# Kernel tuning notes

Measured on AMD Instinct MI355X. Metric: run time of the kernel, lower is better.

## Reference

```python
import jax, jax.numpy as jnp
import numpy as np
import math

B, C, H, W = 16, 256, 128, 128
N = 4096
D = 256  # out_channels
IMG = 512


def _bilinear_sample(features, grid):
    """features (B,C,H,W), grid (B,N,2) in [-1,1] (x,y). align_corners=True, border padding."""
    Bq, Cq, Hq, Wq = features.shape
    ix = (grid[..., 0] + 1.0) * 0.5 * (Wq - 1)  # (B,N)
    iy = (grid[..., 1] + 1.0) * 0.5 * (Hq - 1)
    # border padding: clamp continuous coords into valid range
    ix = jnp.clip(ix, 0.0, Wq - 1)
    iy = jnp.clip(iy, 0.0, Hq - 1)
    x0 = jnp.floor(ix)
    y0 = jnp.floor(iy)
    wx = ix - x0
    wy = iy - y0
    x0i = jnp.clip(x0.astype(jnp.int32), 0, Wq - 1)
    y0i = jnp.clip(y0.astype(jnp.int32), 0, Hq - 1)
    x1i = jnp.clip(x0i + 1, 0, Wq - 1)
    y1i = jnp.clip(y0i + 1, 0, Hq - 1)
    f = features.reshape(Bq, Cq, Hq * Wq)

    def gather(yi, xi):
        idx = (yi * Wq + xi)[:, None, :]  # (B,1,N)
        return jnp.take_along_axis(f, idx, axis=2)  # (B,C,N)

    v00 = gather(y0i, x0i)
    v01 = gather(y0i, x1i)
    v10 = gather(y1i, x0i)
    v11 = gather(y1i, x1i)
    wx = wx[:, None, :]
    wy = wy[:, None, :]
    top = v00 * (1 - wx) + v01 * wx
    bot = v10 * (1 - wx) + v11 * wx
    return top * (1 - wy) + bot * wy  # (B,C,N)


def _pos_encoding(positions, d_model):
    """positions (B,N,2) in [0,1] -> (B,N,2*d_model) sinusoidal."""
    div_term = jnp.exp(jnp.arange(0, d_model, 2, dtype=jnp.float32)
                       * (-math.log(10000.0) / d_model))  # (d_model//2,)
    x = positions[..., 0:1] * 1000.0  # (B,N,1)
    y = positions[..., 1:2] * 1000.0

    def interleave(v):
        a = v * div_term  # (B,N,d_model//2)
        sc = jnp.stack([jnp.sin(a), jnp.cos(a)], axis=-1)  # (B,N,d//2,2)
        return sc.reshape(*v.shape[:-1], d_model)

    return jnp.concatenate([interleave(x), interleave(y)], axis=-1)


def setup_inputs() -> dict:
    key = jax.random.key(0)
    ks = jax.random.split(key, 8)
    features = jax.random.normal(ks[0], (B, C, H, W), dtype=jnp.float32)
    vertices = jax.random.uniform(ks[1], (B, N, 2), dtype=jnp.float32) * IMG
    s1 = 1.0 / math.sqrt(C)
    s2 = 1.0 / math.sqrt(D)
    W1 = jax.random.uniform(ks[2], (C, D), jnp.float32, -s1, s1)
    b1 = jnp.zeros((D,), jnp.float32)
    W2 = jax.random.uniform(ks[3], (D, D), jnp.float32, -s2, s2)
    b2 = jnp.zeros((D,), jnp.float32)
    Wp = jax.random.uniform(ks[4], (D, D), jnp.float32, -s2, s2)
    bp = jnp.zeros((D,), jnp.float32)
    return {"features": features, "vertices": vertices, "image_size": IMG,
            "W1": W1, "b1": b1, "W2": W2, "b2": b2, "Wp": Wp, "bp": bp}


def reference(features, vertices, image_size, W1, b1, W2, b2, Wp, bp):
    # normalize pixel coords to [-1,1] (align_corners=True convention)
    denom = jnp.float32(image_size - 1)
    grid = 2.0 * vertices / denom - 1.0  # (B,N,2)
    sampled = _bilinear_sample(features, grid)  # (B,C,N)
    sampled = jnp.transpose(sampled, (0, 2, 1))  # (B,N,C)
    h = jax.nn.relu(jnp.einsum('bnc,cd->bnd', sampled, W1) + b1)
    vfeat = jnp.einsum('bnd,de->bne', h, W2) + b2  # (B,N,D)
    pos_enc = _pos_encoding(vertices / jnp.float32(image_size), D // 2)  # (B,N,D)
    out = jnp.einsum('bnd,de->bne', vfeat + pos_enc, Wp) + bp
    return out
```

## Files before the change

### kernel.cpp

```cpp
#include <hip/hip_runtime.h>

#define HW 16384
#define Nn 4096

typedef __bf16 bf16x8 __attribute__((ext_vector_type(8)));
typedef unsigned short us8t __attribute__((ext_vector_type(8)));
typedef float f32x4 __attribute__((ext_vector_type(4)));

__device__ __forceinline__ unsigned short f2bf(float f) {
    unsigned int u = __float_as_uint(f);
    u = (u + 0x7fffu + ((u >> 16) & 1u)) >> 16;
    return (unsigned short)u;
}
__device__ __forceinline__ float bf2f(unsigned int h) {
    return __uint_as_float(h << 16);
}
__device__ __forceinline__ f32x4 mfma16(us8t a, us8t b, f32x4 c) {
    return __builtin_amdgcn_mfma_f32_16x16x32_bf16(
        __builtin_bit_cast(bf16x8, a), __builtin_bit_cast(bf16x8, b), c, 0, 0, 0);
}

__global__ __launch_bounds__(256) void k_wt(const float* __restrict__ W1,
                                            const float* __restrict__ W2,
                                            const float* __restrict__ Wp,
                                            unsigned short* __restrict__ WT) {
    const int m = blockIdx.x >> 8;
    const int d = blockIdx.x & 255;
    const int c = threadIdx.x;
    const float* W = (m == 0) ? W1 : (m == 1) ? W2 : Wp;
    WT[m * 65536 + d * 256 + c] = f2bf(W[c * 256 + d]);
}

__global__ __launch_bounds__(256) void k_gemm1(const float* __restrict__ f,
                                               const unsigned short* __restrict__ W1T,
                                               unsigned short* __restrict__ S, int b0) {
    __shared__ __align__(16) unsigned short Asb[64][40];

    const int blk = blockIdx.x;
    const int bl = blk >> 8;
    const int b = b0 + bl;
    const int p0 = (blk & 255) << 6;
    const int t = threadIdx.x;
    const int lane = t & 63;
    const int w = t >> 6;
    const int sc = t >> 4;
    const int sp = (t & 15) << 2;
    const int mrow = lane & 15;
    const int kg = (lane >> 4) << 3;
    const int n0w = w << 6;

    const float* fb = f + ((size_t)b << 22);

    f32x4 acc[4][4];
#pragma unroll
    for (int i = 0; i < 4; ++i)
#pragma unroll
        for (int j = 0; j < 4; ++j) acc[i][j] = (f32x4){0.f, 0.f, 0.f, 0.f};

    us8t bnx[4];
#pragma unroll
    for (int nt = 0; nt < 4; ++nt)
        bnx[nt] = *(const us8t*)(W1T + ((n0w + (nt << 4) + mrow) << 8) + kg);

    for (int k0 = 0; k0 < 256; k0 += 32) {
        __syncthreads();
#pragma unroll
        for (int it = 0; it < 2; ++it) {
            const int c = sc + (it << 4);
            const float4 v = *(const float4*)(fb + ((size_t)(k0 + c) << 14) + p0 + sp);
            Asb[sp + 0][c] = f2bf(v.x);
            Asb[sp + 1][c] = f2bf(v.y);
            Asb[sp + 2][c] = f2bf(v.z);
            Asb[sp + 3][c] = f2bf(v.w);
        }
        us8t bcur[4];
#pragma unroll
        for (int nt = 0; nt < 4; ++nt) bcur[nt] = bnx[nt];
        if (k0 < 224) {
#pragma unroll
            for (int nt = 0; nt < 4; ++nt)
                bnx[nt] = *(const us8t*)(W1T + ((n0w + (nt << 4) + mrow) << 8) + k0 + 32 + kg);
        }
        __syncthreads();
        us8t af[4];
#pragma unroll
        for (int mt = 0; mt < 4; ++mt)
            af[mt] = *(const us8t*)&Asb[(mt << 4) + mrow][kg];
#pragma unroll
        for (int mt = 0; mt < 4; ++mt)
#pragma unroll
            for (int nt = 0; nt < 4; ++nt)
                acc[mt][nt] = mfma16(af[mt], bcur[nt], acc[mt][nt]);
    }

    unsigned short* Sp = S + ((((size_t)bl << 14) + p0) << 8);
    const int r0 = (lane >> 4) << 2;
#pragma unroll
    for (int mt = 0; mt < 4; ++mt)
#pragma unroll
        for (int nt = 0; nt < 4; ++nt) {
            const int col = n0w + (nt << 4) + mrow;
#pragma unroll
            for (int j = 0; j < 4; ++j) {
                const int row = (mt << 4) + r0 + j;
                Sp[((size_t)row << 8) + col] = f2bf(acc[mt][nt][j]);
            }
        }
}

__global__ __launch_bounds__(256) void k_fused(const unsigned short* __restrict__ S,
                                               const float* __restrict__ verts,
                                               const int* __restrict__ iszp,
                                               const unsigned short* __restrict__ W2T,
                                               const unsigned short* __restrict__ WpT,
                                               const float* __restrict__ b1,
                                               const float* __restrict__ b2,
                                               const float* __restrict__ bpv,
                                               float* __restrict__ out, int b0) {
    __shared__ __align__(16) unsigned short hT[64][264];
    __shared__ __align__(16) int pIdx[64][4];
    __shared__ __align__(16) float wBl[64][4];
    __shared__ float vps[64][2];
    __shared__ __align__(16) float b1s[256];
    __shared__ float b2s[256], bps[256];

    const int blk = blockIdx.x;
    const int bl = blk >> 6;
    const int b = b0 + bl;
    const int n0 = (blk & 63) << 6;
    const int t = threadIdx.x;
    const int lane = t & 63;
    const int w = t >> 6;

    b1s[t] = b1[t];
    b2s[t] = b2[t];
    bps[t] = bpv[t];

    if (t < 64) {
        const float isz = (float)iszp[0];
        const size_t vo = ((size_t)b * Nn + n0 + t) << 1;
        const float vx = verts[vo + 0];
        const float vy = verts[vo + 1];
        const float gs = 127.0f / (isz - 1.0f);
        const float ix = fminf(fmaxf(vx * gs, 0.0f), 127.0f);
        const float iy = fminf(fmaxf(vy * gs, 0.0f), 127.0f);
        const float x0 = floorf(ix), y0 = floorf(iy);
        const float wx = ix - x0, wy = iy - y0;
        const int x0i = (int)x0, y0i = (int)y0;
        const int x1i = min(x0i + 1, 127), y1i = min(y0i + 1, 127);
        pIdx[t][0] = (y0i << 7) + x0i;
        pIdx[t][1] = (y0i << 7) + x1i;
        pIdx[t][2] = (y1i << 7) + x0i;
        pIdx[t][3] = (y1i << 7) + x1i;
        wBl[t][0] = (1.0f - wx) * (1.0f - wy);
        wBl[t][1] = wx * (1.0f - wy);
        wBl[t][2] = (1.0f - wx) * wy;
        wBl[t][3] = wx * wy;
        vps[t][0] = vx / isz;
        vps[t][1] = vy / isz;
    }
    __syncthreads();

    {
        const unsigned short* Sb = S + ((size_t)bl << 22);
        const float4 bl1 = *(const float4*)&b1s[lane << 2];
        for (int i = 0; i < 16; ++i) {
            const int r = (w << 4) + i;
            const int4 pp = *(const int4*)pIdx[r];
            const float4 wt = *(const float4*)wBl[r];
            const uint2 a0 = *(const uint2*)(Sb + ((size_t)pp.x << 8) + (lane << 2));
            const uint2 a1 = *(const uint2*)(Sb + ((size_t)pp.y << 8) + (lane << 2));
            const uint2 a2 = *(const uint2*)(Sb + ((size_t)pp.z << 8) + (lane << 2));
            const uint2 a3 = *(const uint2*)(Sb + ((size_t)pp.w << 8) + (lane << 2));
            float d0 = wt.x * bf2f(a0.x & 0xffffu) + wt.y * bf2f(a1.x & 0xffffu) +
                       wt.z * bf2f(a2.x & 0xffffu) + wt.w * bf2f(a3.x & 0xffffu) + bl1.x;
            float d1 = wt.x * bf2f(a0.x >> 16) + wt.y * bf2f(a1.x >> 16) +
                       wt.z * bf2f(a2.x >> 16) + wt.w * bf2f(a3.x >> 16) + bl1.y;
            float d2 = wt.x * bf2f(a0.y & 0xffffu) + wt.y * bf2f(a1.y & 0xffffu) +
                       wt.z * bf2f(a2.y & 0xffffu) + wt.w * bf2f(a3.y & 0xffffu) + bl1.z;
            float d3 = wt.x * bf2f(a0.y >> 16) + wt.y * bf2f(a1.y >> 16) +
                       wt.z * bf2f(a2.y >> 16) + wt.w * bf2f(a3.y >> 16) + bl1.w;
            d0 = fmaxf(d0, 0.0f);
            d1 = fmaxf(d1, 0.0f);
            d2 = fmaxf(d2, 0.0f);
            d3 = fmaxf(d3, 0.0f);
            uint2 pk;
            pk.x = (unsigned)f2bf(d0) | ((unsigned)f2bf(d1) << 16);
            pk.y = (unsigned)f2bf(d2) | ((unsigned)f2bf(d3) << 16);
            *(uint2*)&hT[r][lane << 2] = pk;
        }
    }
    __syncthreads();

    const int mrow = lane & 15;
    const int kg = (lane >> 4) << 3;
    const int r0 = (lane >> 4) << 2;
    const int n0w = w << 6;

    f32x4 acc[4][4];
#pragma unroll
    for (int i = 0; i < 4; ++i)
#pragma unroll
        for (int j = 0; j < 4; ++j) acc[i][j] = (f32x4){0.f, 0.f, 0.f, 0.f};

    us8t bnx[4];
#pragma unroll
    for (int nt = 0; nt < 4; ++nt)
        bnx[nt] = *(const us8t*)(W2T + ((n0w + (nt << 4) + mrow) << 8) + kg);
    for (int k0 = 0; k0 < 256; k0 += 32) {
        us8t bcur[4];
#pragma unroll
        for (int nt = 0; nt < 4; ++nt) bcur[nt] = bnx[nt];
        if (k0 < 224) {
#pragma unroll
            for (int nt = 0; nt < 4; ++nt)
                bnx[nt] = *(const us8t*)(W2T + ((n0w + (nt << 4) + mrow) << 8) + k0 + 32 + kg);
        }
        us8t af[4];
#pragma unroll
        for (int mt = 0; mt < 4; ++mt)
            af[mt] = *(const us8t*)&hT[(mt << 4) + mrow][k0 + kg];
#pragma unroll
        for (int mt = 0; mt < 4; ++mt)
#pragma unroll
            for (int nt = 0; nt < 4; ++nt)
                acc[mt][nt] = mfma16(af[mt], bcur[nt], acc[mt][nt]);
    }
    __syncthreads();

    const float C2 = -0.20762050593046f;
#pragma unroll
    for (int nt = 0; nt < 4; ++nt) {
        const int col = n0w + (nt << 4) + mrow;
        const float bias2 = b2s[col];
        const int ci = col & 127;
        const float dv = exp2f((float)(ci >> 1) * C2) * 1000.0f;
        const int sel = col >> 7;
#pragma unroll
        for (int mt = 0; mt < 4; ++mt)
#pragma unroll
            for (int j = 0; j < 4; ++j) {
                const int row = (mt << 4) + r0 + j;
                const float ang = vps[row][sel] * dv;
                const float pe = (col & 1) ? __cosf(ang) : __sinf(ang);
                hT[row][col] = f2bf(acc[mt][nt][j] + bias2 + pe);
            }
    }
    __syncthreads();

#pragma unroll
    for (int i = 0; i < 4; ++i)
#pragma unroll
        for (int j = 0; j < 4; ++j) acc[i][j] = (f32x4){0.f, 0.f, 0.f, 0.f};
#pragma unroll
    for (int nt = 0; nt < 4; ++nt)
        bnx[nt] = *(const us8t*)(WpT + ((n0w + (nt << 4) + mrow) << 8) + kg);
    for (int k0 = 0; k0 < 256; k0 += 32) {
        us8t bcur[4];
#pragma unroll
        for (int nt = 0; nt < 4; ++nt) bcur[nt] = bnx[nt];
        if (k0 < 224) {
#pragma unroll
            for (int nt = 0; nt < 4; ++nt)
                bnx[nt] = *(const us8t*)(WpT + ((n0w + (nt << 4) + mrow) << 8) + k0 + 32 + kg);
        }
        us8t af[4];
#pragma unroll
        for (int mt = 0; mt < 4; ++mt)
            af[mt] = *(const us8t*)&hT[(mt << 4) + mrow][k0 + kg];
#pragma unroll
        for (int mt = 0; mt < 4; ++mt)
#pragma unroll
            for (int nt = 0; nt < 4; ++nt)
                acc[mt][nt] = mfma16(af[mt], bcur[nt], acc[mt][nt]);
    }

    float* ob = out + (((size_t)b * Nn + n0) << 8);
#pragma unroll
    for (int nt = 0; nt < 4; ++nt) {
        const int col = n0w + (nt << 4) + mrow;
        const float bb = bps[col];
#pragma unroll
        for (int mt = 0; mt < 4; ++mt)
#pragma unroll
            for (int j = 0; j < 4; ++j) {
                const int row = (mt << 4) + r0 + j;
                ob[((size_t)row << 8) + col] = acc[mt][nt][j] + bb;
            }
    }
}

extern "C" void kernel_launch(void* const* d_in, const int* in_sizes, int n_in,
                              void* d_out, int out_size, void* d_ws, size_t ws_size,
                              hipStream_t stream) {
    const float* f = (const float*)d_in[0];
    const float* verts = (const float*)d_in[1];
    const int* isz = (const int*)d_in[2];
    const float* W1 = (const float*)d_in[3];
    const float* b1 = (const float*)d_in[4];
    const float* W2 = (const float*)d_in[5];
    const float* b2 = (const float*)d_in[6];
    const float* Wp = (const float*)d_in[7];
    const float* bp = (const float*)d_in[8];
    float* out = (float*)d_out;

    unsigned short* WT = (unsigned short*)d_ws;
    const size_t S_OFF = 512u << 10;
    unsigned short* S = (unsigned short*)((char*)d_ws + S_OFF);

    const size_t perBatch = (size_t)HW * 256 * 2;
    size_t sbytes = (ws_size > S_OFF) ? (ws_size - S_OFF) : 0;
    int nbMax = (int)(sbytes / perBatch);
    if (nbMax < 1) nbMax = 1;
    if (nbMax > 16) nbMax = 16;

    k_wt<<<dim3(768), dim3(256), 0, stream>>>(W1, W2, Wp, WT);
    for (int b0 = 0; b0 < 16; b0 += nbMax) {
        const int nb = (16 - b0 < nbMax) ? (16 - b0) : nbMax;
        k_gemm1<<<dim3(nb * 256), dim3(256), 0, stream>>>(f, WT, S, b0);
        k_fused<<<dim3(nb * 64), dim3(256), 0, stream>>>(S, verts, isz, WT + 65536, WT + 131072,
                                                         b1, b2, bp, out, b0);
    }
}
```

Before: 516.2 us.

## Restructure gemm1 with 32x32 MFMA, double-buffered swizzled LDS and prefetch

Rewrites the first GEMM kernel to use 32x32x16 bf16 MFMA tiles instead of 16x16x32. The A tile now goes through a double-buffered, XOR-swizzled LDS layout with packed 128-bit stores, which drops one barrier per k-step and avoids bank conflicts. Feature values for the next k-step are prefetched into registers, and block indices are remapped across 8 groups to improve locality. The costs are higher accumulator register pressure and less coalesced per-lane scalar global loads, since each lane now reads a single float per channel row.

```diff
diff --git a/kernel.cpp b/kernel.cpp
--- a/kernel.cpp
+++ b/kernel.cpp
@@ -6,6 +6,7 @@
 typedef __bf16 bf16x8 __attribute__((ext_vector_type(8)));
 typedef unsigned short us8t __attribute__((ext_vector_type(8)));
 typedef float f32x4 __attribute__((ext_vector_type(4)));
+typedef float f32x16 __attribute__((ext_vector_type(16)));
 
 __device__ __forceinline__ unsigned short f2bf(float f) {
     unsigned int u = __float_as_uint(f);
@@ -17,6 +18,10 @@
 }
 __device__ __forceinline__ f32x4 mfma16(us8t a, us8t b, f32x4 c) {
     return __builtin_amdgcn_mfma_f32_16x16x32_bf16(
+        __builtin_bit_cast(bf16x8, a), __builtin_bit_cast(bf16x8, b), c, 0, 0, 0);
+}
+__device__ __forceinline__ f32x16 mfma32(us8t a, us8t b, f32x16 c) {
+    return __builtin_amdgcn_mfma_f32_32x32x16_bf16(
         __builtin_bit_cast(bf16x8, a), __builtin_bit_cast(bf16x8, b), c, 0, 0, 0);
 }
 
@@ -34,76 +39,102 @@
 __global__ __launch_bounds__(256) void k_gemm1(const float* __restrict__ f,
                                                const unsigned short* __restrict__ W1T,
                                                unsigned short* __restrict__ S, int b0) {
-    __shared__ __align__(16) unsigned short Asb[64][40];
-
-    const int blk = blockIdx.x;
+    __shared__ __align__(16) unsigned short Asb[2][64][32];
+
+    int blk = blockIdx.x;
+    if ((gridDim.x & 7) == 0) {
+        const int chunk = gridDim.x >> 3;
+        blk = (blk & 7) * chunk + (blk >> 3);
+    }
     const int bl = blk >> 8;
     const int b = b0 + bl;
     const int p0 = (blk & 255) << 6;
     const int t = threadIdx.x;
     const int lane = t & 63;
     const int w = t >> 6;
-    const int sc = t >> 4;
-    const int sp = (t & 15) << 2;
-    const int mrow = lane & 15;
-    const int kg = (lane >> 4) << 3;
-    const int n0w = w << 6;
-
-    const float* fb = f + ((size_t)b << 22);
-
-    f32x4 acc[4][4];
-#pragma unroll
-    for (int i = 0; i < 4; ++i)
-#pragma unroll
-        for (int j = 0; j < 4; ++j) acc[i][j] = (f32x4){0.f, 0.f, 0.f, 0.f};
-
-    us8t bnx[4];
-#pragma unroll
-    for (int nt = 0; nt < 4; ++nt)
-        bnx[nt] = *(const us8t*)(W1T + ((n0w + (nt << 4) + mrow) << 8) + kg);
+    const int l5 = lane >> 5;
+    const int r31 = lane & 31;
+
+    const float* fb = f + ((size_t)b << 22) + p0 + lane;
+
+    unsigned short* wP = &Asb[0][lane][(w ^ ((lane >> 2) & 3)) << 3];
+    const int G = (r31 >> 2) & 3;
+    const unsigned short* rP0 = &Asb[0][r31][(l5 ^ G) << 3];
+    const unsigned short* rP1 = &Asb[0][r31][((2 + l5) ^ G) << 3];
+
+    f32x16 acc[2][2];
+#pragma unroll
+    for (int i = 0; i < 2; ++i)
+#pragma unroll
+        for (int j = 0; j < 2; ++j)
+#pragma unroll
+            for (int r = 0; r < 16; ++r) acc[i][j][r] = 0.f;
+
+    const unsigned short* Bp0 = W1T + (((w << 6) + r31) << 8) + (l5 << 3);
+    const unsigned short* Bp1 = Bp0 + (32 << 8);
+
+    float pf[8];
+#pragma unroll
+    for (int j = 0; j < 8; ++j) pf[j] = fb[(size_t)((w << 3) + j) << 14];
+
+    us8t bnx[2][2];
+    bnx[0][0] = *(const us8t*)(Bp0);
+    bnx[0][1] = *(const us8t*)(Bp0 + 16);
+    bnx[1][0] = *(const us8t*)(Bp1);
+    bnx[1][1] = *(const us8t*)(Bp1 + 16);
 
     for (int k0 = 0; k0 < 256; k0 += 32) {
+        const int bo = ((k0 >> 5) & 1) << 11;
+
+        uint4 pk;
+        pk.x = (unsigned)f2bf(pf[0]) | ((unsigned)f2bf(pf[1]) << 16);
+        pk.y = (unsigned)f2bf(pf[2]) | ((unsigned)f2bf(pf[3]) << 16);
+        pk.z = (unsigned)f2bf(pf[4]) | ((unsigned)f2bf(pf[5]) << 16);
+        pk.w = (unsigned)f2bf(pf[6]) | ((unsigned)f2bf(pf[7]) << 16);
+        *(uint4*)(wP + bo) = pk;
+
+        us8t bcur[2][2];
+        bcur[0][0] = bnx[0][0]; bcur[0][1] = bnx[0][1];
+        bcur[1][0] = bnx[1][0]; bcur[1][1] = bnx[1][1];
+
+        if (k0 < 224) {
+#pragma unroll
+            for (int j = 0; j < 8; ++j)
+                pf[j] = fb[(size_t)(k0 + 32 + (w << 3) + j) << 14];
+            bnx[0][0] = *(const us8t*)(Bp0 + k0 + 32);
+            bnx[0][1] = *(const us8t*)(Bp0 + k0 + 48);
+            bnx[1][0] = *(const us8t*)(Bp1 + k0 + 32);
+            bnx[1][1] = *(const us8t*)(Bp1 + k0 + 48);
+        }
+
         __syncthreads();
-#pragma unroll
-        for (int it = 0; it < 2; ++it) {
-            const int c = sc + (it << 4);
-            const float4 v = *(const float4*)(fb + ((size_t)(k0 + c) << 14) + p0 + sp);
-            Asb[sp + 0][c] = f2bf(v.x);
-            Asb[sp + 1][c] = f2bf(v.y);
-            Asb[sp + 2][c] = f2bf(v.z);
-            Asb[sp + 3][c] = f2bf(v.w);
-        }
-        us8t bcur[4];
-#pragma unroll
-        for (int nt = 0; nt < 4; ++nt) bcur[nt] = bnx[nt];
-        if (k0 < 224) {
-#pragma unroll
-            for (int nt = 0; nt < 4; ++nt)
-                bnx[nt] = *(const us8t*)(W1T + ((n0w + (nt << 4) + mrow) << 8) + k0 + 32 + kg);
-        }
-        __syncthreads();
-        us8t af[4];
-#pragma unroll
-        for (int mt = 0; mt < 4; ++mt)
-            af[mt] = *(const us8t*)&Asb[(mt << 4) + mrow][kg];
-#pragma unroll
-        for (int mt = 0; mt < 4; ++mt)
-#pragma unroll
-            for (int nt = 0; nt < 4; ++nt)
-                acc[mt][nt] = mfma16(af[mt], bcur[nt], acc[mt][nt]);
+
+        us8t af[2][2];
+        af[0][0] = *(const us8t*)(rP0 + bo);
+        af[0][1] = *(const us8t*)(rP1 + bo);
+        af[1][0] = *(const us8t*)(rP0 + bo + 1024);
+        af[1][1] = *(const us8t*)(rP1 + bo + 1024);
+
+#pragma unroll
+        for (int mt = 0; mt < 2; ++mt)
+#pragma unroll
+            for (int nt = 0; nt < 2; ++nt) {
+                acc[mt][nt] = mfma32(af[mt][0], bcur[nt][0], acc[mt][nt]);
+                acc[mt][nt] = mfma32(af[mt][1], bcur[nt][1], acc[mt][nt]);
+            }
     }
 
     unsigned short* Sp = S + ((((size_t)bl << 14) + p0) << 8);
-    const int r0 = (lane >> 4) << 2;
-#pragma unroll
-    for (int mt = 0; mt < 4; ++mt)
-#pragma unroll
-        for (int nt = 0; nt < 4; ++nt) {
-            const int col = n0w + (nt << 4) + mrow;
-#pragma unroll
-            for (int j = 0; j < 4; ++j) {
-                const int row = (mt << 4) + r0 + j;
-                Sp[((size_t)row << 8) + col] = f2bf(acc[mt][nt][j]);
+    const int rbase = l5 << 2;
+#pragma unroll
+    for (int mt = 0; mt < 2; ++mt)
+#pragma unroll
+        for (int nt = 0; nt < 2; ++nt) {
+            const int d = (w << 6) + (nt << 5) + r31;
+#pragma unroll
+            for (int r = 0; r < 16; ++r) {
+                const int row = (mt << 5) + ((r >> 2) << 3) + (r & 3) + rbase;
+                Sp[((size_t)row << 8) + d] = f2bf(acc[mt][nt][r]);
             }
         }
 }
```

Result: no change. 525.4 us (+1.8%).

## Reorder bilinear sampling before first linear layer, replace GEMM1 with transpose

Applied to the files above, without the earlier changes.

Uses the linearity of bilinear sampling to apply W1 after gathering the four neighbours, so the first GEMM runs on sampled points instead of every feature-map pixel. The previous full-map GEMM kernel becomes a plain fp32-to-bf16 transpose into pixel-major layout, and the fused kernel gains an extra MFMA stage with bias and ReLU. This reduces the first layer's FLOPs, but the transpose still moves the full feature map, and bf16 rounding now happens on the sampled features rather than on the projected ones.

```diff
diff --git a/kernel.cpp b/kernel.cpp
--- a/kernel.cpp
+++ b/kernel.cpp
@@ -14,6 +14,9 @@
 }
 __device__ __forceinline__ float bf2f(unsigned int h) {
     return __uint_as_float(h << 16);
+}
+__device__ __forceinline__ unsigned int pack2(unsigned short a, unsigned short b) {
+    return (unsigned)a | ((unsigned)b << 16);
 }
 __device__ __forceinline__ f32x4 mfma16(us8t a, us8t b, f32x4 c) {
     return __builtin_amdgcn_mfma_f32_16x16x32_bf16(
@@ -31,98 +34,73 @@
     WT[m * 65536 + d * 256 + c] = f2bf(W[c * 256 + d]);
 }
 
-__global__ __launch_bounds__(256) void k_gemm1(const float* __restrict__ f,
-                                               const unsigned short* __restrict__ W1T,
-                                               unsigned short* __restrict__ S, int b0) {
-    __shared__ __align__(16) unsigned short Asb[64][40];
-
-    const int blk = blockIdx.x;
+__global__ __launch_bounds__(256) void k_tr(const float* __restrict__ f,
+                                            unsigned short* __restrict__ fT, int b0) {
+    __shared__ __align__(16) unsigned short fsh[64][272];
+
+    int blk = blockIdx.x;
+    if ((gridDim.x & 7) == 0) {
+        const int chunk = gridDim.x >> 3;
+        blk = (blk & 7) * chunk + (blk >> 3);
+    }
     const int bl = blk >> 8;
     const int b = b0 + bl;
-    const int p0 = (blk & 255) << 6;
+    const int j = blk & 255;
+    const int p0 = (j >> 2) << 8;
+    const int c0 = (j & 3) << 6;
     const int t = threadIdx.x;
     const int lane = t & 63;
     const int w = t >> 6;
-    const int sc = t >> 4;
-    const int sp = (t & 15) << 2;
-    const int mrow = lane & 15;
-    const int kg = (lane >> 4) << 3;
-    const int n0w = w << 6;
 
     const float* fb = f + ((size_t)b << 22);
 
-    f32x4 acc[4][4];
-#pragma unroll
-    for (int i = 0; i < 4; ++i)
-#pragma unroll
-        for (int j = 0; j < 4; ++j) acc[i][j] = (f32x4){0.f, 0.f, 0.f, 0.f};
-
-    us8t bnx[4];
-#pragma unroll
-    for (int nt = 0; nt < 4; ++nt)
-        bnx[nt] = *(const us8t*)(W1T + ((n0w + (nt << 4) + mrow) << 8) + kg);
-
-    for (int k0 = 0; k0 < 256; k0 += 32) {
-        __syncthreads();
-#pragma unroll
-        for (int it = 0; it < 2; ++it) {
-            const int c = sc + (it << 4);
-            const float4 v = *(const float4*)(fb + ((size_t)(k0 + c) << 14) + p0 + sp);
-            Asb[sp + 0][c] = f2bf(v.x);
-            Asb[sp + 1][c] = f2bf(v.y);
-            Asb[sp + 2][c] = f2bf(v.z);
-            Asb[sp + 3][c] = f2bf(v.w);
-        }
-        us8t bcur[4];
-#pragma unroll
-        for (int nt = 0; nt < 4; ++nt) bcur[nt] = bnx[nt];
-        if (k0 < 224) {
-#pragma unroll
-            for (int nt = 0; nt < 4; ++nt)
-                bnx[nt] = *(const us8t*)(W1T + ((n0w + (nt << 4) + mrow) << 8) + k0 + 32 + kg);
-        }
-        __syncthreads();
-        us8t af[4];
-#pragma unroll
-        for (int mt = 0; mt < 4; ++mt)
-            af[mt] = *(const us8t*)&Asb[(mt << 4) + mrow][kg];
-#pragma unroll
-        for (int mt = 0; mt < 4; ++mt)
-#pragma unroll
-            for (int nt = 0; nt < 4; ++nt)
-                acc[mt][nt] = mfma16(af[mt], bcur[nt], acc[mt][nt]);
-    }
-
-    unsigned short* Sp = S + ((((size_t)bl << 14) + p0) << 8);
-    const int r0 = (lane >> 4) << 2;
-#pragma unroll
-    for (int mt = 0; mt < 4; ++mt)
-#pragma unroll
-        for (int nt = 0; nt < 4; ++nt) {
-            const int col = n0w + (nt << 4) + mrow;
-#pragma unroll
-            for (int j = 0; j < 4; ++j) {
-                const int row = (mt << 4) + r0 + j;
-                Sp[((size_t)row << 8) + col] = f2bf(acc[mt][nt][j]);
-            }
-        }
-}
-
-__global__ __launch_bounds__(256) void k_fused(const unsigned short* __restrict__ S,
+    float4 v[16];
+#pragma unroll
+    for (int i = 0; i < 16; ++i) {
+        const int c = c0 + (w << 4) + i;
+        v[i] = *(const float4*)(fb + ((size_t)c << 14) + p0 + (lane << 2));
+    }
+#pragma unroll
+    for (int i = 0; i < 16; ++i) {
+        const int cl = (w << 4) + i;
+        unsigned short* d = &fsh[cl][lane << 2];
+        d[0] = f2bf(v[i].x);
+        d[1] = f2bf(v[i].y);
+        d[2] = f2bf(v[i].z);
+        d[3] = f2bf(v[i].w);
+    }
+    __syncthreads();
+
+    unsigned short* orow = fT + ((size_t)bl << 22) + ((size_t)(p0 + t) << 8) + c0;
+#pragma unroll
+    for (int k = 0; k < 8; ++k) {
+        uint4 q;
+        q.x = pack2(fsh[(k << 3) + 0][t], fsh[(k << 3) + 1][t]);
+        q.y = pack2(fsh[(k << 3) + 2][t], fsh[(k << 3) + 3][t]);
+        q.z = pack2(fsh[(k << 3) + 4][t], fsh[(k << 3) + 5][t]);
+        q.w = pack2(fsh[(k << 3) + 6][t], fsh[(k << 3) + 7][t]);
+        *(uint4*)(orow + (k << 3)) = q;
+    }
+}
+
+__global__ __launch_bounds__(256) void k_fused(const unsigned short* __restrict__ fT,
                                                const float* __restrict__ verts,
                                                const int* __restrict__ iszp,
-                                               const unsigned short* __restrict__ W2T,
-                                               const unsigned short* __restrict__ WpT,
+                                               const unsigned short* __restrict__ WT,
                                                const float* __restrict__ b1,
                                                const float* __restrict__ b2,
                                                const float* __restrict__ bpv,
                                                float* __restrict__ out, int b0) {
-    __shared__ __align__(16) unsigned short hT[64][264];
+    __shared__ __align__(16) unsigned short tT[64][264];
     __shared__ __align__(16) int pIdx[64][4];
     __shared__ __align__(16) float wBl[64][4];
     __shared__ float vps[64][2];
     __shared__ __align__(16) float b1s[256];
     __shared__ float b2s[256], bps[256];
+
+    const unsigned short* W1T = WT;
+    const unsigned short* W2T = WT + 65536;
+    const unsigned short* WpT = WT + 131072;
 
     const int blk = blockIdx.x;
     const int bl = blk >> 6;
@@ -162,32 +140,27 @@
     __syncthreads();
 
     {
-        const unsigned short* Sb = S + ((size_t)bl << 22);
-        const float4 bl1 = *(const float4*)&b1s[lane << 2];
+        const unsigned short* Fb = fT + ((size_t)bl << 22);
         for (int i = 0; i < 16; ++i) {
             const int r = (w << 4) + i;
             const int4 pp = *(const int4*)pIdx[r];
             const float4 wt = *(const float4*)wBl[r];
-            const uint2 a0 = *(const uint2*)(Sb + ((size_t)pp.x << 8) + (lane << 2));
-            const uint2 a1 = *(const uint2*)(Sb + ((size_t)pp.y << 8) + (lane << 2));
-            const uint2 a2 = *(const uint2*)(Sb + ((size_t)pp.z << 8) + (lane << 2));
-            const uint2 a3 = *(const uint2*)(Sb + ((size_t)pp.w << 8) + (lane << 2));
-            float d0 = wt.x * bf2f(a0.x & 0xffffu) + wt.y * bf2f(a1.x & 0xffffu) +
-                       wt.z * bf2f(a2.x & 0xffffu) + wt.w * bf2f(a3.x & 0xffffu) + bl1.x;
-            float d1 = wt.x * bf2f(a0.x >> 16) + wt.y * bf2f(a1.x >> 16) +
-                       wt.z * bf2f(a2.x >> 16) + wt.w * bf2f(a3.x >> 16) + bl1.y;
-            float d2 = wt.x * bf2f(a0.y & 0xffffu) + wt.y * bf2f(a1.y & 0xffffu) +
-                       wt.z * bf2f(a2.y & 0xffffu) + wt.w * bf2f(a3.y & 0xffffu) + bl1.z;
-            float d3 = wt.x * bf2f(a0.y >> 16) + wt.y * bf2f(a1.y >> 16) +
-                       wt.z * bf2f(a2.y >> 16) + wt.w * bf2f(a3.y >> 16) + bl1.w;
-            d0 = fmaxf(d0, 0.0f);
-            d1 = fmaxf(d1, 0.0f);
-            d2 = fmaxf(d2, 0.0f);
-            d3 = fmaxf(d3, 0.0f);
+            const uint2 a0 = *(const uint2*)(Fb + ((size_t)pp.x << 8) + (lane << 2));
+            const uint2 a1 = *(const uint2*)(Fb + ((size_t)pp.y << 8) + (lane << 2));
+            const uint2 a2 = *(const uint2*)(Fb + ((size_t)pp.z << 8) + (lane << 2));
+            const uint2 a3 = *(const uint2*)(Fb + ((size_t)pp.w << 8) + (lane << 2));
+            const float d0 = wt.x * bf2f(a0.x & 0xffffu) + wt.y * bf2f(a1.x & 0xffffu) +
+                             wt.z * bf2f(a2.x & 0xffffu) + wt.w * bf2f(a3.x & 0xffffu);
+            const float d1 = wt.x * bf2f(a0.x >> 16) + wt.y * bf2f(a1.x >> 16) +
+                             wt.z * bf2f(a2.x >> 16) + wt.w * bf2f(a3.x >> 16);
+            const float d2 = wt.x * bf2f(a0.y & 0xffffu) + wt.y * bf2f(a1.y & 0xffffu) +
+                             wt.z * bf2f(a2.y & 0xffffu) + wt.w * bf2f(a3.y & 0xffffu);
+            const float d3 = wt.x * bf2f(a0.y >> 16) + wt.y * bf2f(a1.y >> 16) +
+                             wt.z * bf2f(a2.y >> 16) + wt.w * bf2f(a3.y >> 16);
             uint2 pk;
-            pk.x = (unsigned)f2bf(d0) | ((unsigned)f2bf(d1) << 16);
-            pk.y = (unsigned)f2bf(d2) | ((unsigned)f2bf(d3) << 16);
-            *(uint2*)&hT[r][lane << 2] = pk;
+            pk.x = pack2(f2bf(d0), f2bf(d1));
+            pk.y = pack2(f2bf(d2), f2bf(d3));
+            *(uint2*)&tT[r][lane << 2] = pk;
         }
     }
     __syncthreads();
@@ -198,12 +171,54 @@
     const int n0w = w << 6;
 
     f32x4 acc[4][4];
+    us8t bnx[4];
+
 #pragma unroll
     for (int i = 0; i < 4; ++i)
 #pragma unroll
         for (int j = 0; j < 4; ++j) acc[i][j] = (f32x4){0.f, 0.f, 0.f, 0.f};
-
-    us8t bnx[4];
+#pragma unroll
+    for (int nt = 0; nt < 4; ++nt)
+        bnx[nt] = *(const us8t*)(W1T + ((n0w + (nt << 4) + mrow) << 8) + kg);
+    for (int k0 = 0; k0 < 256; k0 += 32) {
+        us8t bcur[4];
+#pragma unroll
+        for (int nt = 0; nt < 4; ++nt) bcur[nt] = bnx[nt];
+        if (k0 < 224) {
+#pragma unroll
+            for (int nt = 0; nt < 4; ++nt)
+                bnx[nt] = *(const us8t*)(W1T + ((n0w + (nt << 4) + mrow) << 8) + k0 + 32 + kg);
+        }
+        us8t af[4];
+#pragma unroll
+        for (int mt = 0; mt < 4; ++mt)
+            af[mt] = *(const us8t*)&tT[(mt << 4) + mrow][k0 + kg];
+#pragma unroll
+        for (int mt = 0; mt < 4; ++mt)
+#pragma unroll
+            for (int nt = 0; nt < 4; ++nt)
+                acc[mt][nt] = mfma16(af[mt], bcur[nt], acc[mt][nt]);
+    }
+    __syncthreads();
+
+#pragma unroll
+    for (int nt = 0; nt < 4; ++nt) {
+        const int col = n0w + (nt << 4) + mrow;
+        const float bb1 = b1s[col];
+#pragma unroll
+        for (int mt = 0; mt < 4; ++mt)
+#pragma unroll
+            for (int j = 0; j < 4; ++j) {
+                const int row = (mt << 4) + r0 + j;
+                tT[row][col] = f2bf(fmaxf(acc[mt][nt][j] + bb1, 0.0f));
+            }
+    }
+    __syncthreads();
+
+#pragma unroll
+    for (int i = 0; i < 4; ++i)
+#pragma unroll
+        for (int j = 0; j < 4; ++j) acc[i][j] = (f32x4){0.f, 0.f, 0.f, 0.f};
 #pragma unroll
     for (int nt = 0; nt < 4; ++nt)
         bnx[nt] = *(const us8t*)(W2T + ((n0w + (nt << 4) + mrow) << 8) + kg);
@@ -219,7 +234,7 @@
         us8t af[4];
 #pragma unroll
         for (int mt = 0; mt < 4; ++mt)
-            af[mt] = *(const us8t*)&hT[(mt << 4) + mrow][k0 + kg];
+            af[mt] = *(const us8t*)&tT[(mt << 4) + mrow][k0 + kg];
 #pragma unroll
         for (int mt = 0; mt < 4; ++mt)
 #pragma unroll
@@ -243,7 +258,7 @@
                 const int row = (mt << 4) + r0 + j;
                 const float ang = vps[row][sel] * dv;
                 const float pe = (col & 1) ? __cosf(ang) : __sinf(ang);
-                hT[row][col] = f2bf(acc[mt][nt][j] + bias2 + pe);
+                tT[row][col] = f2bf(acc[mt][nt][j] + bias2 + pe);
             }
     }
     __syncthreads();
@@ -267,7 +282,7 @@
         us8t af[4];
 #pragma unroll
         for (int mt = 0; mt < 4; ++mt)
-            af[mt] = *(const us8t*)&hT[(mt << 4) + mrow][k0 + kg];
+            af[mt] = *(const us8t*)&tT[(mt << 4) + mrow][k0 + kg];
 #pragma unroll
         for (int mt = 0; mt < 4; ++mt)
 #pragma unroll
@@ -306,7 +321,7 @@
 
     unsigned short* WT = (unsigned short*)d_ws;
     const size_t S_OFF = 512u << 10;
-    unsigned short* S = (unsigned short*)((char*)d_ws + S_OFF);
+    unsigned short* fT = (unsigned short*)((char*)d_ws + S_OFF);
 
     const size_t perBatch = (size_t)HW * 256 * 2;
     size_t sbytes = (ws_size > S_OFF) ? (ws_size - S_OFF) : 0;
@@ -317,8 +332,8 @@
     k_wt<<<dim3(768), dim3(256), 0, stream>>>(W1, W2, Wp, WT);
     for (int b0 = 0; b0 < 16; b0 += nbMax) {
         const int nb = (16 - b0 < nbMax) ? (16 - b0) : nbMax;
-        k_gemm1<<<dim3(nb * 256), dim3(256), 0, stream>>>(f, WT, S, b0);
-        k_fused<<<dim3(nb * 64), dim3(256), 0, stream>>>(S, verts, isz, WT + 65536, WT + 131072,
+        k_tr<<<dim3(nb * 256), dim3(256), 0, stream>>>(f, fT, b0);
+        k_fused<<<dim3(nb * 64), dim3(256), 0, stream>>>(fT, verts, isz, WT,
                                                          b1, b2, bp, out, b0);
     }
 }
```

Result: faster. 489.3 us (-5.2%).
